# Optimization experiments

Hardware: AMD Instinct MI355X
Metric: run time of the kernel (lower is better)

Reference implementation:

```python
import jax, jax.numpy as jnp
import numpy as np

H = 8          # heads
DH = 64        # dim_head
GH = 40        # grid height (sqrt(num_patches))
GW = 40        # grid width
DIS_DEPTH = 96 # default depth used in the distance term of relative_pos_index_dis
N = GH * GW    # num_patches = 1600
DIM = 512
NEG_THRESH = 0.9
GATE = -2.0    # fixed non-trainable gate


def _rel_index_dis():
    gh, gw = jnp.meshgrid(jnp.arange(GH), jnp.arange(GW), indexing='ij')
    flat = jnp.stack([gh.reshape(-1), gw.reshape(-1)])          # [2, N]
    rel = flat[:, :, None] - flat[:, None, :]                   # [2, N, N]
    dh = rel[0].astype(jnp.float32)
    dw = rel[1].astype(jnp.float32)
    # NB: source uses relative_coords[:,:,1] twice (dw appears in both last terms)
    dis = (dh / GH) ** 2 + (dw / GW) ** 2 + (dw / DIS_DEPTH) ** 2
    idx = (rel[0] + GH - 1) * (2 * GW - 1) + (rel[1] + GW - 1)  # [N, N] in [0, (2h-1)(2w-1))
    return idx, dis


def setup_inputs() -> dict:
    key = jax.random.key(0)
    ks = jax.random.split(key, 8)
    x = jax.random.normal(ks[0], (1, N, DIM), jnp.float32)
    # prob < 0.9 everywhere -> all queries selected (static shapes, exact math)
    prob = jax.random.uniform(ks[1], (1, N), jnp.float32) * 0.89
    w_qkv = jax.random.normal(ks[2], (3 * H * DH, DIM), jnp.float32) * 0.02
    tbl = (2 * GH - 1) * (2 * GW - 1)
    table1 = jax.random.normal(ks[3], (tbl, H), jnp.float32) * 0.02
    table2 = jax.random.normal(ks[4], (tbl, H), jnp.float32) * 0.02
    headsita = jnp.arange(1, H + 1, dtype=jnp.float32) * 0.1  # torch.range(1, heads)*0.1
    w_thresh = jax.random.normal(ks[5], (DH,), jnp.float32) * 0.02
    w_out = jax.random.normal(ks[6], (DIM, H * DH), jnp.float32) * 0.02
    b_out = jnp.zeros((DIM,), jnp.float32)
    return {"x": x, "prob": prob, "w_qkv": w_qkv, "table1": table1,
            "table2": table2, "headsita": headsita, "w_thresh": w_thresh,
            "w_out": w_out, "b_out": b_out}


def reference(x, prob, w_qkv, table1, table2, headsita, w_thresh, w_out, b_out):
    B = x.shape[0]  # 1
    qkv = x @ w_qkv.T                                            # [B, N, 3*H*DH]
    q, k, v = jnp.split(qkv, 3, axis=-1)
    resh = lambda t: t.reshape(B, N, H, DH).transpose(0, 2, 1, 3)  # b h n d
    q, k, v = resh(q), resh(k), resh(v)

    sel = prob[0] < NEG_THRESH                                   # [N] bool (all True here)
    scale = DH ** -0.5
    dots0 = jnp.einsum('bhnd,bhmd->bhnm', q, k) * scale          # [B, H, N, N]

    idx, dis = _rel_index_dis()
    # multiplicative combination of the two bias tables, gathered by rel index
    bias = (table1[idx] * table2[idx]).transpose(2, 0, 1)        # [H, N, N]
    factor = 1.0 / (2.0 * headsita ** 2 + 1e-6)                  # [H]
    pos_embed = jnp.exp(-factor[:, None, None] * dis[None])      # [H, N, N]
    dots = dots0 + bias[None] + 0.01 * pos_embed[None]

    attn = jax.nn.softmax(dots, axis=-1)                         # [B, H, N, N]

    # dynamic per-row threshold pruning + renormalization
    a_max = attn.max(axis=-1)                                    # [B, H, N]
    a_min = attn.min(axis=-1)
    thr = jax.nn.sigmoid(jnp.einsum('bhnd,d->bhn', q, w_thresh)) * jax.nn.sigmoid(jnp.float32(GATE))
    thresh = a_min + thr * (a_max - a_min)                       # [B, H, N]
    record = (attn > thresh[..., None]).astype(attn.dtype)
    deno = jnp.einsum('bhnm,bhnm->bhn', attn, record)
    attn_p = attn * record / (deno[..., None] + 1e-6)

    out0 = jnp.einsum('bhnm,bhmd->bhnd', attn_p, v)              # [B, H, N, DH]
    out0 = out0.transpose(0, 2, 1, 3).reshape(B, N, H * DH)
    out0 = out0 @ w_out.T + b_out                                # [B, N, DIM]

    out = jnp.where(sel[None, :, None], out0, 0.0)               # out[:, ~sel] = 0 (x*0)
    attn0 = jax.nn.softmax(dots0, axis=-1)
    return out, attn0
```

## Files before the change

kernel.cpp:

```cpp
#include <hip/hip_runtime.h>

#define NPATCH 1600
#define NHEAD 8
#define DHEAD 64
#define DMODEL 512
#define TBL 6241
#define QKVLD 1536
#define SROW 1608
#define KSLD 65

__global__ __launch_bounds__(256) void k_gemm_qkv(const float* __restrict__ x,
                                                  const float* __restrict__ w,
                                                  float* __restrict__ c,
                                                  int ldc) {
  __shared__ float As[16][68];
  __shared__ float Bs[16][68];
  const int t = threadIdx.x;
  const int m0 = blockIdx.x * 64;
  const int n0 = blockIdx.y * 64;
  const int tx = t & 15;
  const int ty = t >> 4;
  const int mr = t >> 2;
  const int k4 = (t & 3) * 4;
  float acc[4][4] = {};
  for (int k0 = 0; k0 < DMODEL; k0 += 16) {
    float4 a4 = *reinterpret_cast<const float4*>(x + (size_t)(m0 + mr) * DMODEL + k0 + k4);
    float4 b4 = *reinterpret_cast<const float4*>(w + (size_t)(n0 + mr) * DMODEL + k0 + k4);
    As[k4 + 0][mr] = a4.x; As[k4 + 1][mr] = a4.y; As[k4 + 2][mr] = a4.z; As[k4 + 3][mr] = a4.w;
    Bs[k4 + 0][mr] = b4.x; Bs[k4 + 1][mr] = b4.y; Bs[k4 + 2][mr] = b4.z; Bs[k4 + 3][mr] = b4.w;
    __syncthreads();
    const float4* As4 = reinterpret_cast<const float4*>(&As[0][0]);
    const float4* Bs4 = reinterpret_cast<const float4*>(&Bs[0][0]);
#pragma unroll
    for (int kk = 0; kk < 16; ++kk) {
      float4 av = As4[kk * 17 + tx];
      float4 bv = Bs4[kk * 17 + ty];
      acc[0][0] += av.x * bv.x; acc[0][1] += av.x * bv.y; acc[0][2] += av.x * bv.z; acc[0][3] += av.x * bv.w;
      acc[1][0] += av.y * bv.x; acc[1][1] += av.y * bv.y; acc[1][2] += av.y * bv.z; acc[1][3] += av.y * bv.w;
      acc[2][0] += av.z * bv.x; acc[2][1] += av.z * bv.y; acc[2][2] += av.z * bv.z; acc[2][3] += av.z * bv.w;
      acc[3][0] += av.w * bv.x; acc[3][1] += av.w * bv.y; acc[3][2] += av.w * bv.z; acc[3][3] += av.w * bv.w;
    }
    __syncthreads();
  }
#pragma unroll
  for (int i = 0; i < 4; ++i) {
    float4 o;
    o.x = acc[i][0]; o.y = acc[i][1]; o.z = acc[i][2]; o.w = acc[i][3];
    *reinterpret_cast<float4*>(c + (size_t)(m0 + tx * 4 + i) * ldc + n0 + ty * 4) = o;
  }
}

__global__ __launch_bounds__(256) void k_gemm_out(const float* __restrict__ a,
                                                  const float* __restrict__ w,
                                                  const float* __restrict__ bias,
                                                  const float* __restrict__ prob,
                                                  float* __restrict__ outp) {
  __shared__ float As[16][68];
  __shared__ float Bs[16][68];
  const int t = threadIdx.x;
  const int m0 = blockIdx.x * 64;
  const int n0 = blockIdx.y * 64;
  const int tx = t & 15;
  const int ty = t >> 4;
  const int mr = t >> 2;
  const int k4 = (t & 3) * 4;
  float acc[4][4] = {};
  for (int k0 = 0; k0 < DMODEL; k0 += 16) {
    float4 a4 = *reinterpret_cast<const float4*>(a + (size_t)(m0 + mr) * DMODEL + k0 + k4);
    float4 b4 = *reinterpret_cast<const float4*>(w + (size_t)(n0 + mr) * DMODEL + k0 + k4);
    As[k4 + 0][mr] = a4.x; As[k4 + 1][mr] = a4.y; As[k4 + 2][mr] = a4.z; As[k4 + 3][mr] = a4.w;
    Bs[k4 + 0][mr] = b4.x; Bs[k4 + 1][mr] = b4.y; Bs[k4 + 2][mr] = b4.z; Bs[k4 + 3][mr] = b4.w;
    __syncthreads();
    const float4* As4 = reinterpret_cast<const float4*>(&As[0][0]);
    const float4* Bs4 = reinterpret_cast<const float4*>(&Bs[0][0]);
#pragma unroll
    for (int kk = 0; kk < 16; ++kk) {
      float4 av = As4[kk * 17 + tx];
      float4 bv = Bs4[kk * 17 + ty];
      acc[0][0] += av.x * bv.x; acc[0][1] += av.x * bv.y; acc[0][2] += av.x * bv.z; acc[0][3] += av.x * bv.w;
      acc[1][0] += av.y * bv.x; acc[1][1] += av.y * bv.y; acc[1][2] += av.y * bv.z; acc[1][3] += av.y * bv.w;
      acc[2][0] += av.z * bv.x; acc[2][1] += av.z * bv.y; acc[2][2] += av.z * bv.z; acc[2][3] += av.z * bv.w;
      acc[3][0] += av.w * bv.x; acc[3][1] += av.w * bv.y; acc[3][2] += av.w * bv.z; acc[3][3] += av.w * bv.w;
    }
    __syncthreads();
  }
#pragma unroll
  for (int i = 0; i < 4; ++i) {
    const int row = m0 + tx * 4 + i;
    const bool sel = prob[row] < 0.9f;
    float4 o;
    o.x = acc[i][0] + bias[n0 + ty * 4 + 0];
    o.y = acc[i][1] + bias[n0 + ty * 4 + 1];
    o.z = acc[i][2] + bias[n0 + ty * 4 + 2];
    o.w = acc[i][3] + bias[n0 + ty * 4 + 3];
    if (!sel) { o.x = 0.f; o.y = 0.f; o.z = 0.f; o.w = 0.f; }
    *reinterpret_cast<float4*>(outp + (size_t)row * DMODEL + n0 + ty * 4) = o;
  }
}

__global__ void k_tprod(const float* __restrict__ t1, const float* __restrict__ t2,
                        float* __restrict__ tp) {
  const int o = blockIdx.x * 256 + threadIdx.x;
  if (o < NHEAD * TBL) {
    const int h = o / TBL;
    const int i = o - h * TBL;
    tp[o] = t1[i * NHEAD + h] * t2[i * NHEAD + h];
  }
}

__global__ __launch_bounds__(256) void k_attn(const float* __restrict__ qkv,
                                              const float* __restrict__ tprod,
                                              const float* __restrict__ headsita,
                                              const float* __restrict__ w_thresh,
                                              float* __restrict__ attn0,
                                              float* __restrict__ out0) {
  __shared__ float sfull[8 * SROW];
  __shared__ float ks[16 * KSLD * 4];
  __shared__ float qs[8 * 68];
  const int t = threadIdx.x;
  const int h = blockIdx.y;
  const int n0 = blockIdx.x * 8;

#pragma unroll
  for (int rep = 0; rep < 2; ++rep) {
    const int e = t + rep * 256;
    const int r = e >> 6, dd = e & 63;
    qs[r * 68 + dd] = qkv[(size_t)(n0 + r) * QKVLD + h * DHEAD + dd];
  }
  __syncthreads();

  const int m_lane = t & 63;
  const int wv = t >> 6;
  const int rA = wv * 2, rB = rA + 1;
  const int nA = n0 + rA, nB = n0 + rB;

  float thrA, thrB;
  {
    const float wt = w_thresh[m_lane];
    float pA = qs[rA * 68 + m_lane] * wt;
    float pB = qs[rB * 68 + m_lane] * wt;
#pragma unroll
    for (int s = 32; s; s >>= 1) {
      pA += __shfl_xor(pA, s, 64);
      pB += __shfl_xor(pB, s, 64);
    }
    thrA = (1.0f / (1.0f + __expf(-pA))) * 0.11920292202211755f;
    thrB = (1.0f / (1.0f + __expf(-pB))) * 0.11920292202211755f;
  }
  const float hs = headsita[h];
  const float fac = 1.0f / (2.0f * hs * hs + 1e-6f);

  float4* ks4 = reinterpret_cast<float4*>(ks);
  const float4* qs4 = reinterpret_cast<const float4*>(qs);
  const int c4 = t & 15;
  const int krb = t >> 4;
  const float* gK = qkv + DMODEL + h * DHEAD + c4 * 4;

  for (int mc = 0; mc < 25; ++mc) {
    const int mb = mc * 64;
    float4 s0v = *reinterpret_cast<const float4*>(gK + (size_t)(mb + krb) * QKVLD);
    float4 s1v = *reinterpret_cast<const float4*>(gK + (size_t)(mb + krb + 16) * QKVLD);
    float4 s2v = *reinterpret_cast<const float4*>(gK + (size_t)(mb + krb + 32) * QKVLD);
    float4 s3v = *reinterpret_cast<const float4*>(gK + (size_t)(mb + krb + 48) * QKVLD);
    __syncthreads();
    ks4[c4 * KSLD + krb]      = s0v;
    ks4[c4 * KSLD + krb + 16] = s1v;
    ks4[c4 * KSLD + krb + 32] = s2v;
    ks4[c4 * KSLD + krb + 48] = s3v;
    __syncthreads();

    float acc0 = 0.f, acc1 = 0.f;
#pragma unroll
    for (int d4 = 0; d4 < 16; ++d4) {
      const float4 kv = ks4[d4 * KSLD + m_lane];
      const float4 qa = qs4[rA * 17 + d4];
      const float4 qb = qs4[rB * 17 + d4];
      acc0 = fmaf(kv.x, qa.x, acc0); acc0 = fmaf(kv.y, qa.y, acc0);
      acc0 = fmaf(kv.z, qa.z, acc0); acc0 = fmaf(kv.w, qa.w, acc0);
      acc1 = fmaf(kv.x, qb.x, acc1); acc1 = fmaf(kv.y, qb.y, acc1);
      acc1 = fmaf(kv.z, qb.z, acc1); acc1 = fmaf(kv.w, qb.w, acc1);
    }
    sfull[rA * SROW + mb + m_lane] = acc0 * 0.125f;
    sfull[rB * SROW + mb + m_lane] = acc1 * 0.125f;
  }

#pragma unroll
  for (int rr = 0; rr < 2; ++rr) {
    const int r = rA + rr;
    const float* srow = sfull + r * SROW;
    float va[25];
#pragma unroll
    for (int j = 0; j < 25; ++j) va[j] = srow[j * 64 + m_lane];
    float mx = -3.4e38f;
#pragma unroll
    for (int j = 0; j < 25; ++j) mx = fmaxf(mx, va[j]);
#pragma unroll
    for (int s = 32; s; s >>= 1) mx = fmaxf(mx, __shfl_xor(mx, s, 64));
    float sm = 0.f;
#pragma unroll
    for (int j = 0; j < 25; ++j) { va[j] = __expf(va[j] - mx); sm += va[j]; }
#pragma unroll
    for (int s = 32; s; s >>= 1) sm += __shfl_xor(sm, s, 64);
    const float inv = 1.0f / sm;
    float* prow = attn0 + (size_t)(h * NPATCH + n0 + r) * NPATCH;
#pragma unroll
    for (int j = 0; j < 25; ++j) prow[j * 64 + m_lane] = va[j] * inv;
  }

#pragma unroll
  for (int rr = 0; rr < 2; ++rr) {
    const int r = rA + rr;
    const int n = n0 + r;
    const int nh = n / 40, nw = n % 40;
    const float thr = rr ? thrB : thrA;
    float* srow = sfull + r * SROW;
    float vb[25];
#pragma unroll
    for (int j = 0; j < 25; ++j) {
      const int m = j * 64 + m_lane;
      const int mh = m / 40, mw = m - mh * 40;
      const int dh = nh - mh, dw = nw - mw;
      const float fdh = (float)dh * 0.025f;
      const float fdwa = (float)dw * 0.025f;
      const float fdwb = (float)dw * (1.0f / 96.0f);
      const float dis = fdh * fdh + fdwa * fdwa + fdwb * fdwb;
      const float bias = tprod[h * TBL + (dh + 39) * 79 + (dw + 39)];
      vb[j] = srow[m] + bias + 0.01f * __expf(-fac * dis);
    }
    float mx = -3.4e38f;
#pragma unroll
    for (int j = 0; j < 25; ++j) mx = fmaxf(mx, vb[j]);
#pragma unroll
    for (int s = 32; s; s >>= 1) mx = fmaxf(mx, __shfl_xor(mx, s, 64));
    float sm = 0.f, mn = 3.4e38f;
#pragma unroll
    for (int j = 0; j < 25; ++j) {
      vb[j] = __expf(vb[j] - mx);
      sm += vb[j];
      mn = fminf(mn, vb[j]);
    }
#pragma unroll
    for (int s = 32; s; s >>= 1) {
      sm += __shfl_xor(sm, s, 64);
      mn = fminf(mn, __shfl_xor(mn, s, 64));
    }
    const float T = mn + thr * (1.0f - mn);
    float ld = 0.f;
#pragma unroll
    for (int j = 0; j < 25; ++j) { if (vb[j] > T) ld += vb[j]; }
#pragma unroll
    for (int s = 32; s; s >>= 1) ld += __shfl_xor(ld, s, 64);
    const float sc = 1.0f / (ld + 1e-6f * sm);
#pragma unroll
    for (int j = 0; j < 25; ++j)
      srow[j * 64 + m_lane] = (vb[j] > T) ? vb[j] * sc : 0.f;
  }
  __syncthreads();

  const int d = t & 63;
  const int g = t >> 6;
  float acc[8] = {0.f, 0.f, 0.f, 0.f, 0.f, 0.f, 0.f, 0.f};
  const float* vcol = qkv + 2 * DMODEL + h * DHEAD + d;
  const float4* sf4 = reinterpret_cast<const float4*>(sfull);
  for (int m = g * 400; m < g * 400 + 400; m += 4) {
    const float v0 = vcol[(size_t)(m + 0) * QKVLD];
    const float v1 = vcol[(size_t)(m + 1) * QKVLD];
    const float v2 = vcol[(size_t)(m + 2) * QKVLD];
    const float v3 = vcol[(size_t)(m + 3) * QKVLD];
#pragma unroll
    for (int r = 0; r < 8; ++r) {
      const float4 ap = sf4[r * 402 + (m >> 2)];
      acc[r] = fmaf(ap.x, v0, acc[r]);
      acc[r] = fmaf(ap.y, v1, acc[r]);
      acc[r] = fmaf(ap.z, v2, acc[r]);
      acc[r] = fmaf(ap.w, v3, acc[r]);
    }
  }
  float* part = ks;
#pragma unroll
  for (int r = 0; r < 8; ++r) part[(g * 8 + r) * 64 + d] = acc[r];
  __syncthreads();
#pragma unroll
  for (int rep = 0; rep < 2; ++rep) {
    const int e = t + rep * 256;
    const int r = e >> 6, dd = e & 63;
    const float s = part[(0 + r) * 64 + dd] + part[(8 + r) * 64 + dd] +
                    part[(16 + r) * 64 + dd] + part[(24 + r) * 64 + dd];
    out0[(size_t)(n0 + r) * DMODEL + h * DHEAD + dd] = s;
  }
}

extern "C" void kernel_launch(void* const* d_in, const int* in_sizes, int n_in,
                              void* d_out, int out_size, void* d_ws, size_t ws_size,
                              hipStream_t stream) {
  const float* x        = (const float*)d_in[0];
  const float* prob     = (const float*)d_in[1];
  const float* w_qkv    = (const float*)d_in[2];
  const float* table1   = (const float*)d_in[3];
  const float* table2   = (const float*)d_in[4];
  const float* headsita = (const float*)d_in[5];
  const float* w_thresh = (const float*)d_in[6];
  const float* w_out    = (const float*)d_in[7];
  const float* b_out    = (const float*)d_in[8];

  float* out   = (float*)d_out;
  float* attn0 = out + (size_t)NPATCH * DMODEL;

  float* qkvb  = (float*)d_ws;
  float* out0b = qkvb + (size_t)NPATCH * QKVLD;
  float* tpb   = out0b + (size_t)NPATCH * DMODEL;

  k_gemm_qkv<<<dim3(25, 24), 256, 0, stream>>>(x, w_qkv, qkvb, QKVLD);
  k_tprod<<<dim3((NHEAD * TBL + 255) / 256), 256, 0, stream>>>(table1, table2, tpb);
  k_attn<<<dim3(200, NHEAD), 256, 0, stream>>>(qkvb, tpb, headsita, w_thresh, attn0, out0b);
  k_gemm_out<<<dim3(25, 8), 256, 0, stream>>>(out0b, w_out, b_out, prob, out);
}
```

Baseline: 422.8 us.

## Keep scores in registers and store pruned probabilities as fp16 in LDS

The raw score rows now stay in per-thread register arrays instead of a full fp32 shared-memory buffer, and only the pruned, renormalized probabilities are written to LDS, in half precision. This roughly halves the LDS footprint so more blocks can be resident per CU (launch bounds now ask for 3 blocks). The P·V loop reads eight fp16 values per LDS access. The costs are higher register pressure, recomputation of exp in the attn0 pass, and fp16 rounding of the probabilities used for the output.

```diff
diff --git a/kernel.cpp b/kernel.cpp
--- a/kernel.cpp
+++ b/kernel.cpp
@@ -1,4 +1,5 @@
 #include <hip/hip_runtime.h>
+#include <hip/hip_fp16.h>
 
 #define NPATCH 1600
 #define NHEAD 8
@@ -6,8 +7,8 @@
 #define DMODEL 512
 #define TBL 6241
 #define QKVLD 1536
-#define SROW 1608
 #define KSLD 65
+#define PHROW 1608
 
 __global__ __launch_bounds__(256) void k_gemm_qkv(const float* __restrict__ x,
                                                   const float* __restrict__ w,
@@ -108,15 +109,15 @@
   }
 }
 
-__global__ __launch_bounds__(256) void k_attn(const float* __restrict__ qkv,
-                                              const float* __restrict__ tprod,
-                                              const float* __restrict__ headsita,
-                                              const float* __restrict__ w_thresh,
-                                              float* __restrict__ attn0,
-                                              float* __restrict__ out0) {
-  __shared__ float sfull[8 * SROW];
+__global__ __launch_bounds__(256, 3) void k_attn(const float* __restrict__ qkv,
+                                                 const float* __restrict__ tprod,
+                                                 const float* __restrict__ headsita,
+                                                 const float* __restrict__ w_thresh,
+                                                 float* __restrict__ attn0,
+                                                 float* __restrict__ out0) {
   __shared__ float ks[16 * KSLD * 4];
   __shared__ float qs[8 * 68];
+  __shared__ _Float16 ph[8 * PHROW];
   const int t = threadIdx.x;
   const int h = blockIdx.y;
   const int n0 = blockIdx.x * 8;
@@ -132,7 +133,6 @@
   const int m_lane = t & 63;
   const int wv = t >> 6;
   const int rA = wv * 2, rB = rA + 1;
-  const int nA = n0 + rA, nB = n0 + rB;
 
   float thrA, thrB;
   {
@@ -150,12 +150,14 @@
   const float hs = headsita[h];
   const float fac = 1.0f / (2.0f * hs * hs + 1e-6f);
 
+  float ra0[25], ra1[25];
   float4* ks4 = reinterpret_cast<float4*>(ks);
   const float4* qs4 = reinterpret_cast<const float4*>(qs);
   const int c4 = t & 15;
   const int krb = t >> 4;
   const float* gK = qkv + DMODEL + h * DHEAD + c4 * 4;
 
+#pragma unroll
   for (int mc = 0; mc < 25; ++mc) {
     const int mb = mc * 64;
     float4 s0v = *reinterpret_cast<const float4*>(gK + (size_t)(mb + krb) * QKVLD);
@@ -180,100 +182,85 @@
       acc1 = fmaf(kv.x, qb.x, acc1); acc1 = fmaf(kv.y, qb.y, acc1);
       acc1 = fmaf(kv.z, qb.z, acc1); acc1 = fmaf(kv.w, qb.w, acc1);
     }
-    sfull[rA * SROW + mb + m_lane] = acc0 * 0.125f;
-    sfull[rB * SROW + mb + m_lane] = acc1 * 0.125f;
-  }
-
-#pragma unroll
-  for (int rr = 0; rr < 2; ++rr) {
-    const int r = rA + rr;
-    const float* srow = sfull + r * SROW;
-    float va[25];
-#pragma unroll
-    for (int j = 0; j < 25; ++j) va[j] = srow[j * 64 + m_lane];
-    float mx = -3.4e38f;
-#pragma unroll
-    for (int j = 0; j < 25; ++j) mx = fmaxf(mx, va[j]);
-#pragma unroll
-    for (int s = 32; s; s >>= 1) mx = fmaxf(mx, __shfl_xor(mx, s, 64));
-    float sm = 0.f;
-#pragma unroll
-    for (int j = 0; j < 25; ++j) { va[j] = __expf(va[j] - mx); sm += va[j]; }
-#pragma unroll
-    for (int s = 32; s; s >>= 1) sm += __shfl_xor(sm, s, 64);
-    const float inv = 1.0f / sm;
-    float* prow = attn0 + (size_t)(h * NPATCH + n0 + r) * NPATCH;
-#pragma unroll
-    for (int j = 0; j < 25; ++j) prow[j * 64 + m_lane] = va[j] * inv;
-  }
-
-#pragma unroll
-  for (int rr = 0; rr < 2; ++rr) {
-    const int r = rA + rr;
-    const int n = n0 + r;
-    const int nh = n / 40, nw = n % 40;
-    const float thr = rr ? thrB : thrA;
-    float* srow = sfull + r * SROW;
-    float vb[25];
-#pragma unroll
-    for (int j = 0; j < 25; ++j) {
-      const int m = j * 64 + m_lane;
-      const int mh = m / 40, mw = m - mh * 40;
-      const int dh = nh - mh, dw = nw - mw;
-      const float fdh = (float)dh * 0.025f;
-      const float fdwa = (float)dw * 0.025f;
-      const float fdwb = (float)dw * (1.0f / 96.0f);
-      const float dis = fdh * fdh + fdwa * fdwa + fdwb * fdwb;
-      const float bias = tprod[h * TBL + (dh + 39) * 79 + (dw + 39)];
-      vb[j] = srow[m] + bias + 0.01f * __expf(-fac * dis);
-    }
-    float mx = -3.4e38f;
-#pragma unroll
-    for (int j = 0; j < 25; ++j) mx = fmaxf(mx, vb[j]);
-#pragma unroll
-    for (int s = 32; s; s >>= 1) mx = fmaxf(mx, __shfl_xor(mx, s, 64));
-    float sm = 0.f, mn = 3.4e38f;
-#pragma unroll
-    for (int j = 0; j < 25; ++j) {
-      vb[j] = __expf(vb[j] - mx);
-      sm += vb[j];
-      mn = fminf(mn, vb[j]);
-    }
-#pragma unroll
-    for (int s = 32; s; s >>= 1) {
-      sm += __shfl_xor(sm, s, 64);
-      mn = fminf(mn, __shfl_xor(mn, s, 64));
-    }
-    const float T = mn + thr * (1.0f - mn);
-    float ld = 0.f;
-#pragma unroll
-    for (int j = 0; j < 25; ++j) { if (vb[j] > T) ld += vb[j]; }
-#pragma unroll
-    for (int s = 32; s; s >>= 1) ld += __shfl_xor(ld, s, 64);
-    const float sc = 1.0f / (ld + 1e-6f * sm);
-#pragma unroll
-    for (int j = 0; j < 25; ++j)
-      srow[j * 64 + m_lane] = (vb[j] > T) ? vb[j] * sc : 0.f;
-  }
+    ra0[mc] = acc0 * 0.125f;
+    ra1[mc] = acc1 * 0.125f;
+  }
+
+#define ATTN0_ROW(RA, ROW)                                                      \
+  {                                                                             \
+    float mx = -3.4e38f;                                                        \
+    _Pragma("unroll") for (int j = 0; j < 25; ++j) mx = fmaxf(mx, RA[j]);       \
+    _Pragma("unroll") for (int s = 32; s; s >>= 1) mx = fmaxf(mx, __shfl_xor(mx, s, 64)); \
+    float sm = 0.f;                                                             \
+    _Pragma("unroll") for (int j = 0; j < 25; ++j) sm += __expf(RA[j] - mx);    \
+    _Pragma("unroll") for (int s = 32; s; s >>= 1) sm += __shfl_xor(sm, s, 64); \
+    const float inv = 1.0f / sm;                                                \
+    float* prow = attn0 + (size_t)(h * NPATCH + n0 + (ROW)) * NPATCH;           \
+    _Pragma("unroll") for (int j = 0; j < 25; ++j)                              \
+      prow[j * 64 + m_lane] = __expf(RA[j] - mx) * inv;                         \
+  }
+  ATTN0_ROW(ra0, rA)
+  ATTN0_ROW(ra1, rB)
+#undef ATTN0_ROW
+
+#define PRUNE_ROW(RA, ROW, THR)                                                 \
+  {                                                                             \
+    const int n = n0 + (ROW);                                                   \
+    const int nh = n / 40, nw = n % 40;                                         \
+    _Pragma("unroll") for (int j = 0; j < 25; ++j) {                            \
+      const int m = j * 64 + m_lane;                                            \
+      const int mh = m / 40, mw = m - mh * 40;                                  \
+      const int dh = nh - mh, dw = nw - mw;                                     \
+      const float fdh = (float)dh * 0.025f;                                     \
+      const float fdwa = (float)dw * 0.025f;                                    \
+      const float fdwb = (float)dw * (1.0f / 96.0f);                            \
+      const float dis = fdh * fdh + fdwa * fdwa + fdwb * fdwb;                  \
+      const float bias = tprod[h * TBL + (dh + 39) * 79 + (dw + 39)];           \
+      RA[j] = RA[j] + bias + 0.01f * __expf(-fac * dis);                        \
+    }                                                                           \
+    float mx = -3.4e38f;                                                        \
+    _Pragma("unroll") for (int j = 0; j < 25; ++j) mx = fmaxf(mx, RA[j]);       \
+    _Pragma("unroll") for (int s = 32; s; s >>= 1) mx = fmaxf(mx, __shfl_xor(mx, s, 64)); \
+    float sm = 0.f, mn = 3.4e38f;                                               \
+    _Pragma("unroll") for (int j = 0; j < 25; ++j) {                            \
+      RA[j] = __expf(RA[j] - mx);                                               \
+      sm += RA[j];                                                              \
+      mn = fminf(mn, RA[j]);                                                    \
+    }                                                                           \
+    _Pragma("unroll") for (int s = 32; s; s >>= 1) {                            \
+      sm += __shfl_xor(sm, s, 64);                                              \
+      mn = fminf(mn, __shfl_xor(mn, s, 64));                                    \
+    }                                                                           \
+    const float T = mn + (THR) * (1.0f - mn);                                   \
+    float ld = 0.f;                                                             \
+    _Pragma("unroll") for (int j = 0; j < 25; ++j) { if (RA[j] > T) ld += RA[j]; } \
+    _Pragma("unroll") for (int s = 32; s; s >>= 1) ld += __shfl_xor(ld, s, 64); \
+    const float sc = 1.0f / (ld + 1e-6f * sm);                                  \
+    _Float16* hrow = ph + (ROW) * PHROW;                                        \
+    _Pragma("unroll") for (int j = 0; j < 25; ++j)                              \
+      hrow[j * 64 + m_lane] = (_Float16)((RA[j] > T) ? RA[j] * sc : 0.f);       \
+  }
+  PRUNE_ROW(ra0, rA, thrA)
+  PRUNE_ROW(ra1, rB, thrB)
+#undef PRUNE_ROW
+
   __syncthreads();
 
   const int d = t & 63;
   const int g = t >> 6;
   float acc[8] = {0.f, 0.f, 0.f, 0.f, 0.f, 0.f, 0.f, 0.f};
   const float* vcol = qkv + 2 * DMODEL + h * DHEAD + d;
-  const float4* sf4 = reinterpret_cast<const float4*>(sfull);
-  for (int m = g * 400; m < g * 400 + 400; m += 4) {
-    const float v0 = vcol[(size_t)(m + 0) * QKVLD];
-    const float v1 = vcol[(size_t)(m + 1) * QKVLD];
-    const float v2 = vcol[(size_t)(m + 2) * QKVLD];
-    const float v3 = vcol[(size_t)(m + 3) * QKVLD];
+  const float4* ph4 = reinterpret_cast<const float4*>(ph);
+  for (int m = g * 400; m < g * 400 + 400; m += 8) {
+    float v[8];
+#pragma unroll
+    for (int i = 0; i < 8; ++i) v[i] = vcol[(size_t)(m + i) * QKVLD];
 #pragma unroll
     for (int r = 0; r < 8; ++r) {
-      const float4 ap = sf4[r * 402 + (m >> 2)];
-      acc[r] = fmaf(ap.x, v0, acc[r]);
-      acc[r] = fmaf(ap.y, v1, acc[r]);
-      acc[r] = fmaf(ap.z, v2, acc[r]);
-      acc[r] = fmaf(ap.w, v3, acc[r]);
+      const float4 raw = ph4[(r * PHROW + m) >> 3];
+      const _Float16* hp = reinterpret_cast<const _Float16*>(&raw);
+#pragma unroll
+      for (int i = 0; i < 8; ++i) acc[r] = fmaf((float)hp[i], v[i], acc[r]);
     }
   }
   float* part = ks;
```

New measurement: 378.3 us. -10.5%, faster.
